# Performance work log

Hardware: AMD Instinct MI355X
Metric: run time of the kernel (lower is better)

Reference implementation:

```python
import jax, jax.numpy as jnp
import numpy as np


def _area2d(a, b, c):
    # signed parallelogram area; broadcasts (b may be a [S,S,2] grid)
    return (b[..., 0] - a[..., 0]) * (c[..., 1] - a[..., 1]) - (b[..., 1] - a[..., 1]) * (c[..., 0] - a[..., 0])


def _lookup_table(size):
    # matches torch: meshgrid(ij) of linspace(-1,1), stack [xx,yy], rot90
    lin = jnp.linspace(-1.0, 1.0, size, dtype=jnp.float32)
    xx, yy = jnp.meshgrid(lin, lin, indexing='ij')
    t = jnp.stack([xx, yy], axis=-1)
    return jnp.rot90(t, 1)  # [S,S,2] screen-space (x,y) per pixel


def _grid_sample(img, grid):
    # bilinear, zeros padding, align_corners=True (old 4-arg ATen grid_sampler_2d)
    C, H, W = img.shape
    x = (grid[..., 0] + 1.0) * 0.5 * (W - 1)
    y = (grid[..., 1] + 1.0) * 0.5 * (H - 1)
    x0 = jnp.floor(x)
    y0 = jnp.floor(y)
    wx = x - x0
    wy = y - y0

    def gather(ix, iy):
        inb = (ix >= 0) & (ix <= W - 1) & (iy >= 0) & (iy <= H - 1)
        ii = jnp.clip(ix, 0, W - 1).astype(jnp.int32)
        jj = jnp.clip(iy, 0, H - 1).astype(jnp.int32)
        return img[:, jj, ii] * inb[None].astype(img.dtype)  # [C,h,w]

    v00 = gather(x0, y0)
    v10 = gather(x0 + 1, y0)
    v01 = gather(x0, y0 + 1)
    v11 = gather(x0 + 1, y0 + 1)
    return (v00 * ((1 - wx) * (1 - wy))[None] + v10 * (wx * (1 - wy))[None]
            + v01 * ((1 - wx) * wy)[None] + v11 * (wx * wy)[None])


def _render(tris, uvs, uvmap, size):
    S = size
    pts = _lookup_table(S)            # [S,S,2]
    uvs_v = uvs * 2.0 - 1.0           # module maps uvs from [0,1] to [-1,1]
    zmin = jnp.min(tris.reshape(-1, 3), axis=0)[2]
    zbuf0 = jnp.full((S, S), zmin, dtype=tris.dtype)
    res0 = jnp.zeros((4, S, S), dtype=tris.dtype)

    def step(carry, tu):
        zbuf, res = carry
        tri, uv = tu                  # tri [3,3], uv [3,2]
        t2 = tri[:, :2]
        w = _area2d(t2[0], t2[1], t2[2])
        valid = w >= 1e-9             # degenerate triangle -> skipped (masked out)
        ws = jnp.where(valid, w, 1.0)
        pAB = _area2d(t2[1], pts, t2[0])
        pCB = _area2d(t2[2], pts, t2[1])
        pCA = _area2d(t2[0], pts, t2[2])
        inside = (jnp.maximum(pAB, 0.0) * jnp.maximum(pCB, 0.0) * jnp.maximum(pCA, 0.0) > 0) & valid
        w1 = pCB / ws
        w2 = pCA / ws
        w3 = 1.0 - w1 - w2
        pts3d = w1[..., None] * tri[0] + w2[..., None] * tri[1] + w3[..., None] * tri[2]  # [S,S,3]
        z = pts3d[..., 2]
        zmsk = z >= zbuf
        ptsUV = w1[..., None] * uv[0] + w2[..., None] * uv[1] + w3[..., None] * uv[2]      # [S,S,2]
        rgb = _grid_sample(uvmap, ptsUV)[:3]  # [3,S,S]
        rmsk = inside & zmsk
        zbuf = jnp.where(rmsk, z, zbuf)
        res = jnp.concatenate([jnp.where(rmsk[None], rgb, res[:3]),
                               jnp.where(rmsk, 1.0, res[3])[None]], axis=0)
        return (zbuf, res), None

    (_, res), _ = jax.lax.scan(step, (zbuf0, res0), (tris, uvs_v))
    return res


def setup_inputs():
    key = jax.random.key(0)
    k1, k2, k3 = jax.random.split(key, 3)
    tris = jax.random.uniform(k1, (256, 3, 3), jnp.float32, -1.0, 1.0)
    uvs = jax.random.uniform(k2, (256, 3, 2), jnp.float32)
    uvmap = jax.random.uniform(k3, (3, 1024, 1024), jnp.float32)
    return {"tris": tris, "uvs": uvs, "uvmap": uvmap, "size": 256}


def reference(tris, uvs, uvmap, size):
    return _render(tris, uvs, uvmap, size)
```

## Files before the change

### kernel.cpp

```cpp
#include <hip/hip_runtime.h>


#define S 256
#define TMAX 256
#define NC 8
#define BT 1024
#define HALF 128
#define MARGIN 0.02f

__global__ __launch_bounds__(BT) void render_kernel(
    const float* __restrict__ tris,
    const float* __restrict__ uvs,
    const float* __restrict__ uvmap,
    float* __restrict__ out,
    int T)
{
#pragma clang fp contract(off)
    __shared__ float4 sd[TMAX][4];
    __shared__ float  zred[TMAX];
    __shared__ int    list[TMAX];
    __shared__ unsigned long long masks[4];
    __shared__ int    woff[5];
    __shared__ float4 cand[NC][HALF];

    const int tid  = threadIdx.x;
    const int bid  = blockIdx.x;
    const int row  = bid >> 1;
    const int half = bid & 1;
    const int j    = half * HALF + (tid & (HALF - 1));
    const int c    = tid >> 7;

    const float px = (float)(-1.0 + (double)j * (2.0 / 255.0));
    const float py = (float)(-1.0 + (double)(S - 1 - row) * (2.0 / 255.0));

    bool keep = false;
    if (tid < TMAX) {
        if (tid < T) {
            const float* p = tris + tid * 9;
            float Ax = p[0], Ay = p[1], Az = p[2];
            float Bx = p[3], By = p[4], Bz = p[5];
            float Cx = p[6], Cy = p[7], Cz = p[8];
            float w = (Bx - Ax) * (Cy - Ay) - (By - Ay) * (Cx - Ax);
            bool valid = (w >= 1e-9f);
            sd[tid][0] = make_float4(Bx, By, Ay - By, Ax - Bx);
            sd[tid][1] = make_float4(Cx, Cy, By - Cy, Bx - Cx);
            sd[tid][2] = make_float4(Ax, Ay, Cy - Ay, Cx - Ax);
            sd[tid][3] = make_float4(valid ? w : 1.0f, Az, Bz, Cz);
            zred[tid] = fminf(Az, fminf(Bz, Cz));
            float ymn = fminf(Ay, fminf(By, Cy));
            float ymx = fmaxf(Ay, fmaxf(By, Cy));
            keep = valid && (py >= ymn - MARGIN) && (py <= ymx + MARGIN);
        } else {
            zred[tid] = 3.0e38f;
        }
    }
    unsigned long long m = __ballot(keep);
    if (tid < TMAX && (tid & 63) == 0) masks[tid >> 6] = m;
    __syncthreads();

    if (tid == 512) {
        int s = 0;
        #pragma unroll
        for (int k = 0; k < 4; ++k) { woff[k] = s; s += __popcll(masks[k]); }
        woff[4] = s;
    }
    for (int s = TMAX / 2; s > 0; s >>= 1) {
        if (tid < s) zred[tid] = fminf(zred[tid], zred[tid + s]);
        __syncthreads();
    }
    if (tid < TMAX && keep) {
        int lane = tid & 63;
        int wv   = tid >> 6;
        int pos  = woff[wv] + __popcll(masks[wv] & ((1ull << lane) - 1ull));
        list[pos] = tid;
    }
    __syncthreads();

    const float zmin  = zred[0];
    const int   nlive = woff[4];

    const int cs = (nlive + NC - 1) / NC;
    const int tb = c * cs;
    const int te = (tb + cs < nlive) ? (tb + cs) : nlive;

    float zcur = zmin;
    int win = -1;
    float w1w = 0.0f, w2w = 0.0f;

    for (int it = tb; it < te; ++it) {
        int tt = list[it];
        float4 r0 = sd[tt][0];
        float4 r1 = sd[tt][1];
        float4 r2 = sd[tt][2];
        float4 r3 = sd[tt][3];
        float pAB = (px - r0.x) * r0.z - (py - r0.y) * r0.w;
        float pCB = (px - r1.x) * r1.z - (py - r1.y) * r1.w;
        float pCA = (px - r2.x) * r2.z - (py - r2.y) * r2.w;
        float prod = fmaxf(pAB, 0.0f) * fmaxf(pCB, 0.0f) * fmaxf(pCA, 0.0f);
        if (prod > 0.0f) {
            float w1 = pCB / r3.x;
            float w2 = pCA / r3.x;
            float w3 = (1.0f - w1) - w2;
            float z = (w1 * r3.y + w2 * r3.z) + w3 * r3.w;
            if (z >= zcur) { zcur = z; win = tt; w1w = w1; w2w = w2; }
        }
    }
    cand[c][tid & (HALF - 1)] = make_float4(zcur, w1w, w2w, (float)win);
    __syncthreads();

    if (tid < HALF) {
        float zb = 0.0f, w1 = 0.0f, w2 = 0.0f;
        int w = -1;
        #pragma unroll
        for (int k = 0; k < NC; ++k) {
            float4 ck = cand[k][tid];
            int cw = (int)ck.w;
            if (cw >= 0 && (w < 0 || ck.x >= zb)) {
                zb = ck.x; w1 = ck.y; w2 = ck.z; w = cw;
            }
        }

        float r = 0.0f, g = 0.0f, b = 0.0f, a = 0.0f;
        if (w >= 0) {
            a = 1.0f;
            float w3 = (1.0f - w1) - w2;
            const float* q = uvs + w * 6;
            float u0x = q[0] * 2.0f - 1.0f, u0y = q[1] * 2.0f - 1.0f;
            float u1x = q[2] * 2.0f - 1.0f, u1y = q[3] * 2.0f - 1.0f;
            float u2x = q[4] * 2.0f - 1.0f, u2y = q[5] * 2.0f - 1.0f;
            float ux = (w1 * u0x + w2 * u1x) + w3 * u2x;
            float uy = (w1 * u0y + w2 * u1y) + w3 * u2y;
            float X = ((ux + 1.0f) * 0.5f) * 1023.0f;
            float Y = ((uy + 1.0f) * 0.5f) * 1023.0f;
            float x0 = floorf(X), y0 = floorf(Y);
            float wx = X - x0, wy = Y - y0;
            float w00 = (1.0f - wx) * (1.0f - wy);
            float w10 = wx * (1.0f - wy);
            float w01 = (1.0f - wx) * wy;
            float w11 = wx * wy;
            float xs1 = x0 + 1.0f, ys1 = y0 + 1.0f;
            bool xin0 = (x0  >= 0.0f) && (x0  <= 1023.0f);
            bool xin1 = (xs1 >= 0.0f) && (xs1 <= 1023.0f);
            bool yin0 = (y0  >= 0.0f) && (y0  <= 1023.0f);
            bool yin1 = (ys1 >= 0.0f) && (ys1 <= 1023.0f);
            int xi0 = (int)fminf(fmaxf(x0,  0.0f), 1023.0f);
            int xi1 = (int)fminf(fmaxf(xs1, 0.0f), 1023.0f);
            int yi0 = (int)fminf(fmaxf(y0,  0.0f), 1023.0f);
            int yi1 = (int)fminf(fmaxf(ys1, 0.0f), 1023.0f);
            float acc[3];
            #pragma unroll
            for (int ch = 0; ch < 3; ++ch) {
                const float* img = uvmap + ch * (1024 * 1024);
                float v00 = (xin0 && yin0) ? img[yi0 * 1024 + xi0] : 0.0f;
                float v10 = (xin1 && yin0) ? img[yi0 * 1024 + xi1] : 0.0f;
                float v01 = (xin0 && yin1) ? img[yi1 * 1024 + xi0] : 0.0f;
                float v11 = (xin1 && yin1) ? img[yi1 * 1024 + xi1] : 0.0f;
                acc[ch] = ((v00 * w00 + v10 * w10) + v01 * w01) + v11 * w11;
            }
            r = acc[0]; g = acc[1]; b = acc[2];
        }

        const int base = row * S + j;
        out[0 * S * S + base] = r;
        out[1 * S * S + base] = g;
        out[2 * S * S + base] = b;
        out[3 * S * S + base] = a;
    }
}

extern "C" void kernel_launch(void* const* d_in, const int* in_sizes, int n_in,
                              void* d_out, int out_size, void* d_ws, size_t ws_size,
                              hipStream_t stream) {
    const float* tris  = (const float*)d_in[0];
    const float* uvs   = (const float*)d_in[1];
    const float* uvmap = (const float*)d_in[2];
    float* out = (float*)d_out;
    int T = in_sizes[0] / 9;
    if (T > TMAX) T = TMAX;
    render_kernel<<<dim3(2 * S), dim3(BT), 0, stream>>>(tris, uvs, uvmap, out, T);
}
```

Measured before the change: 78.27 us.

## Cull triangles by x-range per half-row and use wave-shuffle zmin reduction

Adds an x bounding-box test against the pixel span covered by each block's half row, so triangles that cannot touch those pixels are dropped from the per-block list. The shared-memory tree reduction for zmin, which needed eight barriers, is replaced with a wave shuffle reduction plus a four-entry partial array. The prefix offsets are now computed redundantly by every thread from popcounts, which removes a serial single-thread step and one barrier. This cuts the per-pixel loop work and the setup synchronisation, at the cost of a few extra ALU ops per thread.

```diff
diff --git a/kernel.cpp b/kernel.cpp
--- a/kernel.cpp
+++ b/kernel.cpp
@@ -17,10 +17,9 @@
 {
 #pragma clang fp contract(off)
     __shared__ float4 sd[TMAX][4];
-    __shared__ float  zred[TMAX];
     __shared__ int    list[TMAX];
     __shared__ unsigned long long masks[4];
-    __shared__ int    woff[5];
+    __shared__ float  zpart[4];
     __shared__ float4 cand[NC][HALF];
 
     const int tid  = threadIdx.x;
@@ -32,52 +31,54 @@
 
     const float px = (float)(-1.0 + (double)j * (2.0 / 255.0));
     const float py = (float)(-1.0 + (double)(S - 1 - row) * (2.0 / 255.0));
+    const float pxlo = (float)(-1.0 + (double)(half * HALF) * (2.0 / 255.0));
+    const float pxhi = (float)(-1.0 + (double)(half * HALF + HALF - 1) * (2.0 / 255.0));
 
     bool keep = false;
-    if (tid < TMAX) {
-        if (tid < T) {
-            const float* p = tris + tid * 9;
-            float Ax = p[0], Ay = p[1], Az = p[2];
-            float Bx = p[3], By = p[4], Bz = p[5];
-            float Cx = p[6], Cy = p[7], Cz = p[8];
-            float w = (Bx - Ax) * (Cy - Ay) - (By - Ay) * (Cx - Ax);
-            bool valid = (w >= 1e-9f);
-            sd[tid][0] = make_float4(Bx, By, Ay - By, Ax - Bx);
-            sd[tid][1] = make_float4(Cx, Cy, By - Cy, Bx - Cx);
-            sd[tid][2] = make_float4(Ax, Ay, Cy - Ay, Cx - Ax);
-            sd[tid][3] = make_float4(valid ? w : 1.0f, Az, Bz, Cz);
-            zred[tid] = fminf(Az, fminf(Bz, Cz));
-            float ymn = fminf(Ay, fminf(By, Cy));
-            float ymx = fmaxf(Ay, fmaxf(By, Cy));
-            keep = valid && (py >= ymn - MARGIN) && (py <= ymx + MARGIN);
-        } else {
-            zred[tid] = 3.0e38f;
-        }
+    float zl = 3.0e38f;
+    if (tid < TMAX && tid < T) {
+        const float* p = tris + tid * 9;
+        float Ax = p[0], Ay = p[1], Az = p[2];
+        float Bx = p[3], By = p[4], Bz = p[5];
+        float Cx = p[6], Cy = p[7], Cz = p[8];
+        float w = (Bx - Ax) * (Cy - Ay) - (By - Ay) * (Cx - Ax);
+        bool valid = (w >= 1e-9f);
+        sd[tid][0] = make_float4(Bx, By, Ay - By, Ax - Bx);
+        sd[tid][1] = make_float4(Cx, Cy, By - Cy, Bx - Cx);
+        sd[tid][2] = make_float4(Ax, Ay, Cy - Ay, Cx - Ax);
+        sd[tid][3] = make_float4(valid ? w : 1.0f, Az, Bz, Cz);
+        zl = fminf(Az, fminf(Bz, Cz));
+        float ymn = fminf(Ay, fminf(By, Cy));
+        float ymx = fmaxf(Ay, fmaxf(By, Cy));
+        float xmn = fminf(Ax, fminf(Bx, Cx));
+        float xmx = fmaxf(Ax, fmaxf(Bx, Cx));
+        keep = valid && (py >= ymn - MARGIN) && (py <= ymx + MARGIN)
+                     && (pxhi >= xmn - MARGIN) && (pxlo <= xmx + MARGIN);
     }
     unsigned long long m = __ballot(keep);
-    if (tid < TMAX && (tid & 63) == 0) masks[tid >> 6] = m;
+    if (tid < TMAX) {
+        float zw = zl;
+        #pragma unroll
+        for (int o = 32; o > 0; o >>= 1) zw = fminf(zw, __shfl_xor(zw, o, 64));
+        if ((tid & 63) == 0) { masks[tid >> 6] = m; zpart[tid >> 6] = zw; }
+    }
     __syncthreads();
 
-    if (tid == 512) {
-        int s = 0;
-        #pragma unroll
-        for (int k = 0; k < 4; ++k) { woff[k] = s; s += __popcll(masks[k]); }
-        woff[4] = s;
-    }
-    for (int s = TMAX / 2; s > 0; s >>= 1) {
-        if (tid < s) zred[tid] = fminf(zred[tid], zred[tid + s]);
-        __syncthreads();
-    }
+    int n0 = __popcll(masks[0]);
+    int n1 = __popcll(masks[1]);
+    int n2 = __popcll(masks[2]);
+    int n3 = __popcll(masks[3]);
+    const int nlive = n0 + n1 + n2 + n3;
+    const float zmin = fminf(fminf(zpart[0], zpart[1]), fminf(zpart[2], zpart[3]));
+
     if (tid < TMAX && keep) {
         int lane = tid & 63;
         int wv   = tid >> 6;
-        int pos  = woff[wv] + __popcll(masks[wv] & ((1ull << lane) - 1ull));
+        int off  = (wv > 0 ? n0 : 0) + (wv > 1 ? n1 : 0) + (wv > 2 ? n2 : 0);
+        int pos  = off + __popcll(masks[wv] & ((1ull << lane) - 1ull));
         list[pos] = tid;
     }
     __syncthreads();
-
-    const float zmin  = zred[0];
-    const int   nlive = woff[4];
 
     const int cs = (nlive + NC - 1) / NC;
     const int tb = c * cs;
```

Result: no change. 76.78 us (-1.9%).
